# Kernel optimization log

Measured on AMD Instinct MI355X. Metric: run time of the kernel, lower is better.

The kernel has to match this reference:

```python
import jax, jax.numpy as jnp
import numpy as np

N_NODES = 50000
N_EDGES = 800000
IN_FEATS = 32
OUT_FEATS = 32
NUM_HEADS = 4


def setup_inputs() -> dict:
    key = jax.random.key(0)
    ks = jax.random.split(key, 12)
    H, F, IN = NUM_HEADS, OUT_FEATS, IN_FEATS
    h = jax.random.normal(ks[0], (N_NODES, IN), dtype=jnp.float32)
    src = jax.random.randint(ks[1], (N_EDGES,), 0, N_NODES, dtype=jnp.int64)
    dst = jax.random.randint(ks[2], (N_EDGES,), 0, N_NODES, dtype=jnp.int64)
    s = 0.1
    W_gat = jax.random.normal(ks[3], (IN, H * F), dtype=jnp.float32) * s
    attn_l = jax.random.normal(ks[4], (H, F), dtype=jnp.float32) * s
    attn_r = jax.random.normal(ks[5], (H, F), dtype=jnp.float32) * s
    W_ih = jax.random.normal(ks[6], (3 * F, H * F), dtype=jnp.float32) * s
    W_hh = jax.random.normal(ks[7], (3 * F, F), dtype=jnp.float32) * s
    b_ih = jax.random.normal(ks[8], (3 * F,), dtype=jnp.float32) * s
    b_hh = jax.random.normal(ks[9], (3 * F,), dtype=jnp.float32) * s
    return {"h": h, "W_gat": W_gat, "attn_l": attn_l, "attn_r": attn_r,
            "W_ih": W_ih, "W_hh": W_hh, "b_ih": b_ih, "b_hh": b_hh,
            "src": src, "dst": dst}


def reference(h, W_gat, attn_l, attn_r, W_ih, W_hh, b_ih, b_hh, src, dst):
    N = h.shape[0]
    H, F = attn_l.shape
    # --- GATConv ---
    feat = (h @ W_gat).reshape(N, H, F)                      # (N,H,F)
    el = jnp.einsum('nhf,hf->nh', feat, attn_l)              # (N,H)
    er = jnp.einsum('nhf,hf->nh', feat, attn_r)              # (N,H)
    e = jax.nn.leaky_relu(el[src] + er[dst], 0.2)            # (E,H) edge logits
    emax = jax.ops.segment_max(e, dst, num_segments=N)       # per-dst max (stable)
    ee = jnp.exp(e - emax[dst])
    denom = jax.ops.segment_sum(ee, dst, num_segments=N)
    alpha = ee / denom[dst]                                  # segment softmax (E,H)
    msg = feat[src] * alpha[:, :, None]                      # (E,H,F)
    agg = jax.ops.segment_sum(msg, dst, num_segments=N)      # (N,H,F)
    x = agg.reshape(N, H * F)
    # --- GRUCell (torch semantics, gate order r,z,n) ---
    gi = x @ W_ih.T + b_ih                                   # (N,3F)
    gh = h @ W_hh.T + b_hh                                   # (N,3F)
    i_r, i_z, i_n = jnp.split(gi, 3, axis=1)
    h_r, h_z, h_n = jnp.split(gh, 3, axis=1)
    r = jax.nn.sigmoid(i_r + h_r)
    z = jax.nn.sigmoid(i_z + h_z)
    n = jnp.tanh(i_n + r * h_n)
    h_new = (1.0 - z) * n + z * h
    return jax.nn.elu(h_new)
```

## Files before the change

kernel.cpp:

```cpp
#include <hip/hip_runtime.h>
#include <hip/hip_bf16.h>
#include <cmath>

#define N_NODES 50000
#define N_EDGES 800000
#define CAP 64

#define NBINS 196
#define BIN_CAP 8192
#define CUR_PAD 32

#define WCB_ITEMS (144 * 32)
#define WCB_BLOCKS (WCB_ITEMS / 256)
#define WC_ITEMS (192 * 160)
#define WC_BLOCKS (WC_ITEMS / 256)

#define P1_EPT 8
#define P1_EPB (256 * P1_EPT)
#define P1_BLOCKS ((N_EDGES + P1_EPB - 1) / P1_EPB)
#define FEAT_BLOCKS ((N_NODES / 16 + 3) / 4)

typedef __attribute__((ext_vector_type(8))) short bf16x8;
typedef __attribute__((ext_vector_type(4))) float f32x4;

__device__ inline short bfbits(float x) {
    __hip_bfloat16 t = __float2bfloat16(x);
    return *reinterpret_cast<short*>(&t);
}

__device__ inline unsigned char f32_to_fp8(float x) {
    return (unsigned char)(__builtin_amdgcn_cvt_pk_fp8_f32(x, x, 0, false) & 0xff);
}

__global__ __launch_bounds__(256) void k_prep0(
        const float* __restrict__ Wg, const float* __restrict__ al,
        const float* __restrict__ ar, const float* __restrict__ Wih,
        const float* __restrict__ Whh, __hip_bfloat16* __restrict__ Wcomb,
        __hip_bfloat16* __restrict__ Wc, int* __restrict__ bin_cursor) {
    const int t = threadIdx.x;
    if (blockIdx.x < WCB_BLOCKS) {
        const int idx = blockIdx.x * 256 + t;
        const int row = idx >> 5, k = idx & 31;
        float v = 0.f;
        if (row < 128) {
            v = Wg[k * 128 + row];
        } else if (row < 136) {
            const int hd = (row - 128) & 3;
            const float* a = (row < 132) ? (al + hd * 32) : (ar + hd * 32);
            const float* w = Wg + k * 128 + hd * 32;
#pragma unroll
            for (int f = 0; f < 32; ++f) v = fmaf(w[f], a[f], v);
        }
        Wcomb[idx] = __float2bfloat16(v);
        return;
    }
    if (blockIdx.x < WCB_BLOCKS + WC_BLOCKS) {
        const int idx = (blockIdx.x - WCB_BLOCKS) * 256 + t;
        const int r = idx / 160, k = idx - r * 160;
        float v = 0.f;
        if (r < 96) { if (k < 128) v = Wih[r * 128 + k]; }
        else        { if (k >= 128) v = Whh[(r - 96) * 32 + (k - 128)]; }
        Wc[idx] = __float2bfloat16(v);
        return;
    }
    if (t < NBINS) bin_cursor[t * CUR_PAD] = 0;
}

__global__ __launch_bounds__(256) void k_part(
        const int* __restrict__ src, const int* __restrict__ dst,
        int* __restrict__ bin_cursor, unsigned* __restrict__ bin_buf) {
    const int t = threadIdx.x;
    __shared__ int bcnt[256], bofs[256], cur[256], gbase[256];
    __shared__ int wt4[4];
    __shared__ unsigned stage[P1_EPB];
    bcnt[t] = 0;
    __syncthreads();
    int bn[P1_EPT];
    unsigned pk[P1_EPT];
    const int ebase = blockIdx.x * P1_EPB + t * P1_EPT;
    if (ebase < N_EDGES) {
        int dd[P1_EPT], ss[P1_EPT];
        *(int4*)(dd)     = *(const int4*)(dst + ebase);
        *(int4*)(dd + 4) = *(const int4*)(dst + ebase + 4);
        *(int4*)(ss)     = *(const int4*)(src + ebase);
        *(int4*)(ss + 4) = *(const int4*)(src + ebase + 4);
#pragma unroll
        for (int q = 0; q < P1_EPT; ++q) {
            bn[q] = dd[q] >> 8;
            pk[q] = (unsigned)ss[q] | ((unsigned)(dd[q] & 255) << 16);
            atomicAdd(&bcnt[bn[q]], 1);
        }
    } else {
#pragma unroll
        for (int q = 0; q < P1_EPT; ++q) bn[q] = -1;
    }
    __syncthreads();
    {
        const int wave = t >> 6, lane = t & 63;
        const int vv = bcnt[t];
        int x = vv;
#pragma unroll
        for (int m = 1; m < 64; m <<= 1) {
            const int y = __shfl_up(x, m, 64);
            if (lane >= m) x += y;
        }
        if (lane == 63) wt4[wave] = x;
        __syncthreads();
        int wb = 0;
#pragma unroll
        for (int i = 0; i < 4; ++i) if (i < wave) wb += wt4[i];
        const int off = wb + x - vv;
        bofs[t] = off;
        cur[t] = off;
        gbase[t] = (vv > 0) ? atomicAdd(&bin_cursor[t * CUR_PAD], vv) : 0;
    }
    __syncthreads();
#pragma unroll
    for (int q = 0; q < P1_EPT; ++q)
        if (bn[q] >= 0) stage[atomicAdd(&cur[bn[q]], 1)] = pk[q];
    __syncthreads();
    if (t < NBINS) {
        const int c = bcnt[t], o = bofs[t], g = gbase[t];
        unsigned* bb = bin_buf + (size_t)t * BIN_CAP;
        for (int j = 0; j < c; ++j) {
            const int gi = g + j;
            if (gi < BIN_CAP) bb[gi] = stage[o + j];
        }
    }
}

__global__ __launch_bounds__(256) void k_feat(
        const float* __restrict__ h, const __hip_bfloat16* __restrict__ Wcomb,
        unsigned char* __restrict__ feat, float* __restrict__ el,
        float* __restrict__ er) {
    __shared__ unsigned char sbuf8[4][16][136];
    const int t = threadIdx.x;
    const int lane = t & 63, wave = t >> 6;
    const int li = lane & 15, quad = lane >> 4;
    const int mt = blockIdx.x * 4 + wave;
    if (mt >= N_NODES / 16) return;
    const int m_base = mt * 16;
    bf16x8 a;
    {
        const float4* hp = (const float4*)(h + (size_t)(m_base + li) * 32 + quad * 8);
        const float4 f0 = hp[0], f1 = hp[1];
        a[0] = bfbits(f0.x); a[1] = bfbits(f0.y); a[2] = bfbits(f0.z); a[3] = bfbits(f0.w);
        a[4] = bfbits(f1.x); a[5] = bfbits(f1.y); a[6] = bfbits(f1.z); a[7] = bfbits(f1.w);
    }
    f32x4 acc[9];
#pragma unroll
    for (int j = 0; j < 9; ++j) acc[j] = (f32x4){0.f, 0.f, 0.f, 0.f};
#pragma unroll
    for (int j = 0; j < 9; ++j) {
        const bf16x8 b = *(const bf16x8*)(Wcomb + (size_t)(j * 16 + li) * 32 + quad * 8);
        acc[j] = __builtin_amdgcn_mfma_f32_16x16x32_bf16(a, b, acc[j], 0, 0, 0);
    }
#pragma unroll
    for (int j = 0; j < 8; ++j)
#pragma unroll
        for (int i = 0; i < 4; ++i)
            sbuf8[wave][quad * 4 + i][j * 16 + li] = f32_to_fp8(acc[j][i]);
    __builtin_amdgcn_wave_barrier();
#pragma unroll
    for (int rep = 0; rep < 4; ++rep) {
        const int row = rep * 4 + quad;
        const unsigned long long v = *(const unsigned long long*)(&sbuf8[wave][row][li * 8]);
        *(unsigned long long*)(feat + (size_t)(m_base + row) * 128 + li * 8) = v;
    }
    if (li < 8) {
#pragma unroll
        for (int i = 0; i < 4; ++i) {
            const int m = m_base + quad * 4 + i;
            if (li < 4) el[m * 4 + li] = acc[8][i];
            else        er[m * 4 + (li - 4)] = acc[8][i];
        }
    }
}

__global__ __launch_bounds__(256) void k_scat2(
        const int* __restrict__ bin_cursor, const unsigned* __restrict__ bin_buf,
        int* __restrict__ srcs_p, int* __restrict__ counts) {
    __shared__ int lcnt[256];
    const int t = threadIdx.x;
    const int b = blockIdx.x;
    lcnt[t] = 0;
    __syncthreads();
    const int cb = min(bin_cursor[b * CUR_PAD], BIN_CAP);
    const uint4* bb4 = (const uint4*)(bin_buf + (size_t)b * BIN_CAP);
    for (int i = t * 4; i < cb; i += 1024) {
        const uint4 p4 = bb4[i >> 2];
#pragma unroll
        for (int k = 0; k < 4; ++k) {
            if (i + k < cb) {
                const unsigned p = (&p4.x)[k];
                const int dl = p >> 16;
                const int s = p & 0xffff;
                const int pos = atomicAdd(&lcnt[dl], 1);
                if (pos < CAP) srcs_p[(size_t)(b * 256 + dl) * CAP + pos] = s;
            }
        }
    }
    __syncthreads();
    const int node = b * 256 + t;
    if (node < N_NODES) counts[node] = lcnt[t];
}

__global__ __launch_bounds__(256) void k_aggr_gru(
        const int* __restrict__ counts, const int* __restrict__ srcs_p,
        const unsigned char* __restrict__ feat,
        const float* __restrict__ el, const float* __restrict__ er,
        const float* __restrict__ h, const __hip_bfloat16* __restrict__ Wc,
        const float* __restrict__ bih, const float* __restrict__ bhh,
        float* __restrict__ out) {
    __shared__ __hip_bfloat16 xh_tile[16][160];
    __shared__ int   sl_s[4][4][64];
    __shared__ float eel_s[4][256];
    __shared__ float ex[2][3][16][16];
    const int wave = threadIdx.x >> 6;
    const int lane = threadIdx.x & 63;
    float* eel = eel_s[wave];
    const int hs = lane & 3;
    const int eh = lane >> 5;
    const int fl = lane & 31;
    const int hq = fl >> 3;
    const int mbase = blockIdx.x * 16;

    int cnts[4];
#pragma unroll
    for (int u = 0; u < 4; ++u) {
        const int n = mbase + wave * 4 + u;
        cnts[u] = min(counts[n], CAP);
        if (lane < cnts[u]) sl_s[wave][u][lane] = srcs_p[(size_t)n * CAP + lane];
    }
    __builtin_amdgcn_wave_barrier();
    for (int u = 0; u < 4; ++u) {
        const int row = wave * 4 + u;
        const int n = mbase + row;
        const float ern = er[n * 4 + hs];
        const int cnt = cnts[u];
        const int* sl = sl_s[wave][u];
        float a0 = 0.f, a1 = 0.f, a2 = 0.f, a3 = 0.f, psum = 0.f;
#pragma unroll
        for (int p = 0; p < 4; ++p) {
            const int j = p * 64 + lane;
            if (j < cnt * 4) {
                const int s = sl[j >> 2];
                float v = el[s * 4 + hs] + ern;
                v = v > 0.f ? v : 0.2f * v;
                const float e = __expf(v);
                eel[j] = e;
                psum += e;
            }
        }
        __builtin_amdgcn_wave_barrier();
        int i = 0;
        for (; i + 8 <= cnt; i += 8) {
            const int s0 = sl[i + eh],     s1 = sl[i + 2 + eh];
            const int s2 = sl[i + 4 + eh], s3 = sl[i + 6 + eh];
            const unsigned u0 = *(const unsigned*)(feat + (size_t)s0 * 128 + fl * 4);
            const unsigned u1 = *(const unsigned*)(feat + (size_t)s1 * 128 + fl * 4);
            const unsigned u2 = *(const unsigned*)(feat + (size_t)s2 * 128 + fl * 4);
            const unsigned u3 = *(const unsigned*)(feat + (size_t)s3 * 128 + fl * 4);
            const float w0 = eel[(i + eh) * 4 + hq];
            const float w1 = eel[(i + 2 + eh) * 4 + hq];
            const float w2 = eel[(i + 4 + eh) * 4 + hq];
            const float w3 = eel[(i + 6 + eh) * 4 + hq];
            a0 = fmaf(w0, __builtin_amdgcn_cvt_f32_fp8(u0, 0), a0);
            a1 = fmaf(w0, __builtin_amdgcn_cvt_f32_fp8(u0, 1), a1);
            a2 = fmaf(w0, __builtin_amdgcn_cvt_f32_fp8(u0, 2), a2);
            a3 = fmaf(w0, __builtin_amdgcn_cvt_f32_fp8(u0, 3), a3);
            a0 = fmaf(w1, __builtin_amdgcn_cvt_f32_fp8(u1, 0), a0);
            a1 = fmaf(w1, __builtin_amdgcn_cvt_f32_fp8(u1, 1), a1);
            a2 = fmaf(w1, __builtin_amdgcn_cvt_f32_fp8(u1, 2), a2);
            a3 = fmaf(w1, __builtin_amdgcn_cvt_f32_fp8(u1, 3), a3);
            a0 = fmaf(w2, __builtin_amdgcn_cvt_f32_fp8(u2, 0), a0);
            a1 = fmaf(w2, __builtin_amdgcn_cvt_f32_fp8(u2, 1), a1);
            a2 = fmaf(w2, __builtin_amdgcn_cvt_f32_fp8(u2, 2), a2);
            a3 = fmaf(w2, __builtin_amdgcn_cvt_f32_fp8(u2, 3), a3);
            a0 = fmaf(w3, __builtin_amdgcn_cvt_f32_fp8(u3, 0), a0);
            a1 = fmaf(w3, __builtin_amdgcn_cvt_f32_fp8(u3, 1), a1);
            a2 = fmaf(w3, __builtin_amdgcn_cvt_f32_fp8(u3, 2), a2);
            a3 = fmaf(w3, __builtin_amdgcn_cvt_f32_fp8(u3, 3), a3);
        }
        for (; i < cnt; i += 2) {
            const int e2 = i + eh;
            if (e2 < cnt) {
                const int s0 = sl[e2];
                const unsigned u0 = *(const unsigned*)(feat + (size_t)s0 * 128 + fl * 4);
                const float w0 = eel[e2 * 4 + hq];
                a0 = fmaf(w0, __builtin_amdgcn_cvt_f32_fp8(u0, 0), a0);
                a1 = fmaf(w0, __builtin_amdgcn_cvt_f32_fp8(u0, 1), a1);
                a2 = fmaf(w0, __builtin_amdgcn_cvt_f32_fp8(u0, 2), a2);
                a3 = fmaf(w0, __builtin_amdgcn_cvt_f32_fp8(u0, 3), a3);
            }
        }
        __builtin_amdgcn_wave_barrier();
        a0 += __shfl_xor(a0, 32, 64);
        a1 += __shfl_xor(a1, 32, 64);
        a2 += __shfl_xor(a2, 32, 64);
        a3 += __shfl_xor(a3, 32, 64);
#pragma unroll
        for (int m = 4; m < 64; m <<= 1) psum += __shfl_xor(psum, m, 64);
        const float dn = __shfl(psum, hq, 64);
        const float inv = (cnt > 0) ? 1.f / dn : 0.f;
        if (lane < 32) {
            __hip_bfloat162 p0, p1;
            p0.x = __float2bfloat16(a0 * inv); p0.y = __float2bfloat16(a1 * inv);
            p1.x = __float2bfloat16(a2 * inv); p1.y = __float2bfloat16(a3 * inv);
            __hip_bfloat162* xp = (__hip_bfloat162*)&xh_tile[row][0];
            xp[lane * 2]     = p0;
            xp[lane * 2 + 1] = p1;
            xh_tile[row][128 + lane] = __float2bfloat16(h[(size_t)n * 32 + lane]);
        }
    }
    __syncthreads();

    const int li = lane & 15, quad = lane >> 4;
    const int cb = wave >> 1;
    const int ghrole = wave & 1;
    bf16x8 a[5];
#pragma unroll
    for (int s = 0; s < 5; ++s)
        a[s] = *(const bf16x8*)((const char*)&xh_tile[0][0] + li * 320 + s * 64 + quad * 16);
    f32x4 acc[3];
#pragma unroll
    for (int g = 0; g < 3; ++g) {
        acc[g] = (f32x4){0.f, 0.f, 0.f, 0.f};
        const int j = g * 2 + cb + ghrole * 6;
        const bf16x8* bp = (const bf16x8*)(Wc + (size_t)(j * 16 + li) * 160 + quad * 8);
        acc[g] = __builtin_amdgcn_mfma_f32_16x16x32_bf16(a[0], bp[0],  acc[g], 0, 0, 0);
        acc[g] = __builtin_amdgcn_mfma_f32_16x16x32_bf16(a[1], bp[4],  acc[g], 0, 0, 0);
        acc[g] = __builtin_amdgcn_mfma_f32_16x16x32_bf16(a[2], bp[8],  acc[g], 0, 0, 0);
        acc[g] = __builtin_amdgcn_mfma_f32_16x16x32_bf16(a[3], bp[12], acc[g], 0, 0, 0);
        acc[g] = __builtin_amdgcn_mfma_f32_16x16x32_bf16(a[4], bp[16], acc[g], 0, 0, 0);
    }
    if (ghrole) {
#pragma unroll
        for (int g = 0; g < 3; ++g)
#pragma unroll
            for (int i = 0; i < 4; ++i)
                ex[cb][g][quad * 4 + i][li] = acc[g][i];
    }
    __syncthreads();
    if (!ghrole) {
        const int c = cb * 16 + li;
        const float bir = bih[c],      bhr = bhh[c];
        const float biz = bih[32 + c], bhz = bhh[32 + c];
        const float bin = bih[64 + c], bhn = bhh[64 + c];
#pragma unroll
        for (int i = 0; i < 4; ++i) {
            const int row = quad * 4 + i;
            const int m = mbase + row;
            const float gr = acc[0][i] + bir + ex[cb][0][row][li] + bhr;
            const float gz = acc[1][i] + biz + ex[cb][1][row][li] + bhz;
            const float r = 1.f / (1.f + expf(-gr));
            const float z = 1.f / (1.f + expf(-gz));
            const float nn = tanhf(acc[2][i] + bin + r * (ex[cb][2][row][li] + bhn));
            const float hv = h[(size_t)m * 32 + c];
            const float hn = (1.f - z) * nn + z * hv;
            out[(size_t)m * 32 + c] = hn > 0.f ? hn : expm1f(hn);
        }
    }
}

extern "C" void kernel_launch(void* const* d_in, const int* in_sizes, int n_in,
                              void* d_out, int out_size, void* d_ws, size_t ws_size,
                              hipStream_t stream) {
    const float* h   = (const float*)d_in[0];
    const float* Wg  = (const float*)d_in[1];
    const float* al  = (const float*)d_in[2];
    const float* ar  = (const float*)d_in[3];
    const float* Wih = (const float*)d_in[4];
    const float* Whh = (const float*)d_in[5];
    const float* bih = (const float*)d_in[6];
    const float* bhh = (const float*)d_in[7];
    const int* src   = (const int*)d_in[8];
    const int* dst   = (const int*)d_in[9];
    float* out = (float*)d_out;

    float* el = (float*)d_ws;
    float* er = el + (size_t)N_NODES * 4;
    unsigned char* feat8 = (unsigned char*)(er + (size_t)N_NODES * 4);
    __hip_bfloat16* Wc    = (__hip_bfloat16*)(feat8 + (size_t)N_NODES * 128);
    __hip_bfloat16* Wcomb = Wc + 192 * 160;
    int* counts  = (int*)(Wcomb + WCB_ITEMS);
    int* srcs_p  = counts + N_NODES;
    int* bin_cursor = srcs_p + (size_t)N_NODES * CAP;
    unsigned* bin_buf = (unsigned*)(bin_cursor + NBINS * CUR_PAD);

    k_prep0<<<WCB_BLOCKS + WC_BLOCKS + 1, 256, 0, stream>>>(
        Wg, al, ar, Wih, Whh, Wcomb, Wc, bin_cursor);
    k_part<<<P1_BLOCKS, 256, 0, stream>>>(src, dst, bin_cursor, bin_buf);
    k_feat<<<FEAT_BLOCKS, 256, 0, stream>>>(h, Wcomb, feat8, el, er);
    k_scat2<<<NBINS, 256, 0, stream>>>(bin_cursor, bin_buf, srcs_p, counts);
    k_aggr_gru<<<N_NODES / 16, 256, 0, stream>>>(
        counts, srcs_p, feat8, el, er, h, Wc, bih, bhh, out);
}
```

Baseline: 156.0 us.

## Fuse edge bucketing into aggregation kernel and merge prep with partition

Removes the separate scatter kernel that built per-node source lists in global memory. Each aggregation block instead rescans its 256-node bin and keeps only the edges belonging to its 16 nodes, building the lists in shared memory. The weight-prep kernel is merged into the partition kernel, which now uses 1024-thread blocks, and the cursor reset becomes a memset. This saves launches and the srcs_p round trip through global memory, at the cost of reading each bin 16 times redundantly. Shared-memory list order now depends on atomics, so the floating-point summation order is nondeterministic.

New measurement: 155.6 us. About the same (-0.3%).

```diff
diff --git a/kernel.cpp b/kernel.cpp
--- a/kernel.cpp
+++ b/kernel.cpp
@@ -11,14 +11,15 @@
 #define CUR_PAD 32
 
 #define WCB_ITEMS (144 * 32)
-#define WCB_BLOCKS (WCB_ITEMS / 256)
 #define WC_ITEMS (192 * 160)
-#define WC_BLOCKS (WC_ITEMS / 256)
-
-#define P1_EPT 8
-#define P1_EPB (256 * P1_EPT)
+#define PREP_ITEMS (WCB_ITEMS + WC_ITEMS)
+#define PREP_BLOCKS ((PREP_ITEMS + 1023) / 1024)
+
+#define P1_EPT 2
+#define P1_EPB (1024 * P1_EPT)
 #define P1_BLOCKS ((N_EDGES + P1_EPB - 1) / P1_EPB)
 #define FEAT_BLOCKS ((N_NODES / 16 + 3) / 4)
+#define AGGR_BLOCKS (N_NODES / 16)
 
 typedef __attribute__((ext_vector_type(8))) short bf16x8;
 typedef __attribute__((ext_vector_type(4))) float f32x4;
@@ -32,92 +33,84 @@
     return (unsigned char)(__builtin_amdgcn_cvt_pk_fp8_f32(x, x, 0, false) & 0xff);
 }
 
-__global__ __launch_bounds__(256) void k_prep0(
+__global__ __launch_bounds__(1024) void k_part_prep(
+        const int* __restrict__ src, const int* __restrict__ dst,
+        int* __restrict__ bin_cursor, unsigned* __restrict__ bin_buf,
         const float* __restrict__ Wg, const float* __restrict__ al,
         const float* __restrict__ ar, const float* __restrict__ Wih,
         const float* __restrict__ Whh, __hip_bfloat16* __restrict__ Wcomb,
-        __hip_bfloat16* __restrict__ Wc, int* __restrict__ bin_cursor) {
+        __hip_bfloat16* __restrict__ Wc) {
     const int t = threadIdx.x;
-    if (blockIdx.x < WCB_BLOCKS) {
-        const int idx = blockIdx.x * 256 + t;
-        const int row = idx >> 5, k = idx & 31;
-        float v = 0.f;
-        if (row < 128) {
-            v = Wg[k * 128 + row];
-        } else if (row < 136) {
-            const int hd = (row - 128) & 3;
-            const float* a = (row < 132) ? (al + hd * 32) : (ar + hd * 32);
-            const float* w = Wg + k * 128 + hd * 32;
-#pragma unroll
-            for (int f = 0; f < 32; ++f) v = fmaf(w[f], a[f], v);
-        }
-        Wcomb[idx] = __float2bfloat16(v);
+    if (blockIdx.x >= P1_BLOCKS) {
+        const int idx = (blockIdx.x - P1_BLOCKS) * 1024 + t;
+        if (idx < WCB_ITEMS) {
+            const int row = idx >> 5, k = idx & 31;
+            float v = 0.f;
+            if (row < 128) {
+                v = Wg[k * 128 + row];
+            } else if (row < 136) {
+                const int hd = (row - 128) & 3;
+                const float* a = (row < 132) ? (al + hd * 32) : (ar + hd * 32);
+                const float* w = Wg + k * 128 + hd * 32;
+#pragma unroll
+                for (int f = 0; f < 32; ++f) v = fmaf(w[f], a[f], v);
+            }
+            Wcomb[idx] = __float2bfloat16(v);
+        } else if (idx < PREP_ITEMS) {
+            const int j = idx - WCB_ITEMS;
+            const int r = j / 160, k = j - r * 160;
+            float v = 0.f;
+            if (r < 96) { if (k < 128) v = Wih[r * 128 + k]; }
+            else        { if (k >= 128) v = Whh[(r - 96) * 32 + (k - 128)]; }
+            Wc[j] = __float2bfloat16(v);
+        }
         return;
     }
-    if (blockIdx.x < WCB_BLOCKS + WC_BLOCKS) {
-        const int idx = (blockIdx.x - WCB_BLOCKS) * 256 + t;
-        const int r = idx / 160, k = idx - r * 160;
-        float v = 0.f;
-        if (r < 96) { if (k < 128) v = Wih[r * 128 + k]; }
-        else        { if (k >= 128) v = Whh[(r - 96) * 32 + (k - 128)]; }
-        Wc[idx] = __float2bfloat16(v);
-        return;
-    }
-    if (t < NBINS) bin_cursor[t * CUR_PAD] = 0;
-}
-
-__global__ __launch_bounds__(256) void k_part(
-        const int* __restrict__ src, const int* __restrict__ dst,
-        int* __restrict__ bin_cursor, unsigned* __restrict__ bin_buf) {
-    const int t = threadIdx.x;
     __shared__ int bcnt[256], bofs[256], cur[256], gbase[256];
     __shared__ int wt4[4];
     __shared__ unsigned stage[P1_EPB];
-    bcnt[t] = 0;
-    __syncthreads();
-    int bn[P1_EPT];
-    unsigned pk[P1_EPT];
-    const int ebase = blockIdx.x * P1_EPB + t * P1_EPT;
+    if (t < 256) bcnt[t] = 0;
+    __syncthreads();
+    int bn0 = -1, bn1 = -1;
+    unsigned pk0 = 0, pk1 = 0;
+    const int ebase = blockIdx.x * P1_EPB + t * 2;
     if (ebase < N_EDGES) {
-        int dd[P1_EPT], ss[P1_EPT];
-        *(int4*)(dd)     = *(const int4*)(dst + ebase);
-        *(int4*)(dd + 4) = *(const int4*)(dst + ebase + 4);
-        *(int4*)(ss)     = *(const int4*)(src + ebase);
-        *(int4*)(ss + 4) = *(const int4*)(src + ebase + 4);
-#pragma unroll
-        for (int q = 0; q < P1_EPT; ++q) {
-            bn[q] = dd[q] >> 8;
-            pk[q] = (unsigned)ss[q] | ((unsigned)(dd[q] & 255) << 16);
-            atomicAdd(&bcnt[bn[q]], 1);
-        }
-    } else {
-#pragma unroll
-        for (int q = 0; q < P1_EPT; ++q) bn[q] = -1;
-    }
-    __syncthreads();
-    {
-        const int wave = t >> 6, lane = t & 63;
-        const int vv = bcnt[t];
-        int x = vv;
+        const int2 dd = *(const int2*)(dst + ebase);
+        const int2 ss = *(const int2*)(src + ebase);
+        bn0 = dd.x >> 8; pk0 = (unsigned)ss.x | ((unsigned)(dd.x & 255) << 16);
+        bn1 = dd.y >> 8; pk1 = (unsigned)ss.y | ((unsigned)(dd.y & 255) << 16);
+        atomicAdd(&bcnt[bn0], 1);
+        atomicAdd(&bcnt[bn1], 1);
+    }
+    __syncthreads();
+    int x = 0, vv = 0;
+    if (t < 256) {
+        vv = bcnt[t];
+        x = vv;
+        const int lane = t & 63;
 #pragma unroll
         for (int m = 1; m < 64; m <<= 1) {
             const int y = __shfl_up(x, m, 64);
             if (lane >= m) x += y;
         }
-        if (lane == 63) wt4[wave] = x;
-        __syncthreads();
+        if (lane == 63) wt4[t >> 6] = x;
+    }
+    __syncthreads();
+    if (t < 256) {
+        const int wave4 = t >> 6;
         int wb = 0;
 #pragma unroll
-        for (int i = 0; i < 4; ++i) if (i < wave) wb += wt4[i];
+        for (int i = 0; i < 4; ++i) if (i < wave4) wb += wt4[i];
         const int off = wb + x - vv;
         bofs[t] = off;
         cur[t] = off;
         gbase[t] = (vv > 0) ? atomicAdd(&bin_cursor[t * CUR_PAD], vv) : 0;
     }
     __syncthreads();
-#pragma unroll
-    for (int q = 0; q < P1_EPT; ++q)
-        if (bn[q] >= 0) stage[atomicAdd(&cur[bn[q]], 1)] = pk[q];
+    if (bn0 >= 0) {
+        stage[atomicAdd(&cur[bn0], 1)] = pk0;
+        stage[atomicAdd(&cur[bn1], 1)] = pk1;
+    }
     __syncthreads();
     if (t < NBINS) {
         const int c = bcnt[t], o = bofs[t], g = gbase[t];
@@ -177,68 +170,57 @@
     }
 }
 
-__global__ __launch_bounds__(256) void k_scat2(
+__global__ __launch_bounds__(256) void k_aggr_gru(
         const int* __restrict__ bin_cursor, const unsigned* __restrict__ bin_buf,
-        int* __restrict__ srcs_p, int* __restrict__ counts) {
-    __shared__ int lcnt[256];
-    const int t = threadIdx.x;
-    const int b = blockIdx.x;
-    lcnt[t] = 0;
-    __syncthreads();
-    const int cb = min(bin_cursor[b * CUR_PAD], BIN_CAP);
-    const uint4* bb4 = (const uint4*)(bin_buf + (size_t)b * BIN_CAP);
-    for (int i = t * 4; i < cb; i += 1024) {
-        const uint4 p4 = bb4[i >> 2];
-#pragma unroll
-        for (int k = 0; k < 4; ++k) {
-            if (i + k < cb) {
-                const unsigned p = (&p4.x)[k];
-                const int dl = p >> 16;
-                const int s = p & 0xffff;
-                const int pos = atomicAdd(&lcnt[dl], 1);
-                if (pos < CAP) srcs_p[(size_t)(b * 256 + dl) * CAP + pos] = s;
-            }
-        }
-    }
-    __syncthreads();
-    const int node = b * 256 + t;
-    if (node < N_NODES) counts[node] = lcnt[t];
-}
-
-__global__ __launch_bounds__(256) void k_aggr_gru(
-        const int* __restrict__ counts, const int* __restrict__ srcs_p,
         const unsigned char* __restrict__ feat,
         const float* __restrict__ el, const float* __restrict__ er,
         const float* __restrict__ h, const __hip_bfloat16* __restrict__ Wc,
         const float* __restrict__ bih, const float* __restrict__ bhh,
         float* __restrict__ out) {
+    __shared__ unsigned short list[16][CAP];
+    __shared__ int lcnt[16];
     __shared__ __hip_bfloat16 xh_tile[16][160];
-    __shared__ int   sl_s[4][4][64];
     __shared__ float eel_s[4][256];
     __shared__ float ex[2][3][16][16];
-    const int wave = threadIdx.x >> 6;
-    const int lane = threadIdx.x & 63;
+    const int t = threadIdx.x;
+    const int wave = t >> 6;
+    const int lane = t & 63;
+    const int pb = blockIdx.x >> 4, six = blockIdx.x & 15;
+    const int mbase = blockIdx.x * 16;
+
+    if (t < 16) lcnt[t] = 0;
+    __syncthreads();
+
+    const int cbn = min(bin_cursor[pb * CUR_PAD], BIN_CAP);
+    const uint4* bb4 = (const uint4*)(bin_buf + (size_t)pb * BIN_CAP);
+    for (int i = t * 4; i < cbn; i += 1024) {
+        const uint4 p4 = bb4[i >> 2];
+#pragma unroll
+        for (int k = 0; k < 4; ++k) {
+            if (i + k < cbn) {
+                const unsigned p = (&p4.x)[k];
+                const int local = (p >> 16) & 255;
+                if ((local >> 4) == six) {
+                    const int dl = local & 15;
+                    const int pos = atomicAdd(&lcnt[dl], 1);
+                    if (pos < CAP) list[dl][pos] = (unsigned short)(p & 0xffff);
+                }
+            }
+        }
+    }
+    __syncthreads();
+
     float* eel = eel_s[wave];
     const int hs = lane & 3;
     const int eh = lane >> 5;
     const int fl = lane & 31;
     const int hq = fl >> 3;
-    const int mbase = blockIdx.x * 16;
-
-    int cnts[4];
-#pragma unroll
-    for (int u = 0; u < 4; ++u) {
-        const int n = mbase + wave * 4 + u;
-        cnts[u] = min(counts[n], CAP);
-        if (lane < cnts[u]) sl_s[wave][u][lane] = srcs_p[(size_t)n * CAP + lane];
-    }
-    __builtin_amdgcn_wave_barrier();
     for (int u = 0; u < 4; ++u) {
         const int row = wave * 4 + u;
         const int n = mbase + row;
         const float ern = er[n * 4 + hs];
-        const int cnt = cnts[u];
-        const int* sl = sl_s[wave][u];
+        const int cnt = min(lcnt[row], CAP);
+        const unsigned short* sl = list[row];
         float a0 = 0.f, a1 = 0.f, a2 = 0.f, a3 = 0.f, psum = 0.f;
 #pragma unroll
         for (int p = 0; p < 4; ++p) {
@@ -382,17 +364,14 @@
     float* er = el + (size_t)N_NODES * 4;
     unsigned char* feat8 = (unsigned char*)(er + (size_t)N_NODES * 4);
     __hip_bfloat16* Wc    = (__hip_bfloat16*)(feat8 + (size_t)N_NODES * 128);
-    __hip_bfloat16* Wcomb = Wc + 192 * 160;
-    int* counts  = (int*)(Wcomb + WCB_ITEMS);
-    int* srcs_p  = counts + N_NODES;
-    int* bin_cursor = srcs_p + (size_t)N_NODES * CAP;
+    __hip_bfloat16* Wcomb = Wc + WC_ITEMS;
+    int* bin_cursor = (int*)(Wcomb + WCB_ITEMS);
     unsigned* bin_buf = (unsigned*)(bin_cursor + NBINS * CUR_PAD);
 
-    k_prep0<<<WCB_BLOCKS + WC_BLOCKS + 1, 256, 0, stream>>>(
-        Wg, al, ar, Wih, Whh, Wcomb, Wc, bin_cursor);
-    k_part<<<P1_BLOCKS, 256, 0, stream>>>(src, dst, bin_cursor, bin_buf);
+    hipMemsetAsync(bin_cursor, 0, NBINS * CUR_PAD * sizeof(int), stream);
+    k_part_prep<<<P1_BLOCKS + PREP_BLOCKS, 1024, 0, stream>>>(
+        src, dst, bin_cursor, bin_buf, Wg, al, ar, Wih, Whh, Wcomb, Wc);
     k_feat<<<FEAT_BLOCKS, 256, 0, stream>>>(h, Wcomb, feat8, el, er);
-    k_scat2<<<NBINS, 256, 0, stream>>>(bin_cursor, bin_buf, srcs_p, counts);
-    k_aggr_gru<<<N_NODES / 16, 256, 0, stream>>>(
-        counts, srcs_p, feat8, el, er, h, Wc, bih, bhh, out);
-}
+    k_aggr_gru<<<AGGR_BLOCKS, 256, 0, stream>>>(
+        bin_cursor, bin_buf, feat8, el, er, h, Wc, bih, bhh, out);
+}
```
